# Kernel tuning notes

Measured on AMD Instinct MI355X. Metric: run time of the kernel, lower is better.

## Reference

```python
import jax, jax.numpy as jnp
import numpy as np

H = 512       # rnn_hidden_dim (enc_units == dec_units)
E = 256       # embedding_dim
V_CN = 32000  # source vocab
V_EN = 32000  # target vocab
B = 64        # batch_size
T_SRC = 64    # max_len_src
T_TRG = 64    # max_len_trg
SOS = 1


def _split3(a):
    return a[..., :H], a[..., H:2 * H], a[..., 2 * H:]


def gru_step(h, x, W, U, b):
    # Keras GRU v2 (reset_after=True), recurrent_activation=sigmoid,
    # activation='sigmoid' (non-standard; replaces tanh in candidate).
    xg = x @ W + b[0]          # [B, 3H]
    hg = h @ U + b[1]          # [B, 3H]
    xz, xr, xh = _split3(xg)
    hz, hr, hh = _split3(hg)
    z = jax.nn.sigmoid(xz + hz)
    r = jax.nn.sigmoid(xr + hr)
    hc = jax.nn.sigmoid(xh + r * hh)
    return z * h + (1.0 - z) * hc


def gru_layer(x, mask, W, U, b, reverse=False):
    # x: [B,T,D], mask: [B,T] bool. Masked steps carry state/output forward (Keras semantics).
    xt = jnp.swapaxes(x, 0, 1)
    mt = jnp.swapaxes(mask, 0, 1)
    if reverse:
        xt = xt[::-1]
        mt = mt[::-1]
    h0 = jnp.zeros((x.shape[0], H), x.dtype)

    def step(h, inp):
        xi, mi = inp
        hn = gru_step(h, xi, W, U, b)
        h = jnp.where(mi[:, None], hn, h)
        return h, h

    hT, ys = jax.lax.scan(step, h0, (xt, mt))
    if reverse:
        ys = ys[::-1]
    return jnp.swapaxes(ys, 0, 1), hT


def setup_inputs() -> dict:
    key = jax.random.key(0)
    ks = iter(jax.random.split(key, 40))

    def p(shape, s=0.05):
        return jax.random.normal(next(ks), shape, jnp.float32) * s

    inp = {
        'src': jax.random.randint(next(ks), (B, T_SRC), 0, V_CN, jnp.int32),
        'trg': jax.random.randint(next(ks), (B, T_TRG), 0, V_EN, jnp.int32),
        # encoder
        'emb_cn': p((V_CN, E)),
        'Wf': p((E, 3 * H)), 'Uf': p((H, 3 * H)), 'bf': p((2, 3 * H)),
        'Wb': p((E, 3 * H)), 'Ub': p((H, 3 * H)), 'bb': p((2, 3 * H)),
        'Wm': p((2 * H, 3 * H)), 'Um': p((H, 3 * H)), 'bm': p((2, 3 * H)),
        'Wt': p((H, 3 * H)), 'Ut': p((H, 3 * H)), 'bt': p((2, 3 * H)),
        # decoder
        'emb_en': p((V_EN, E)),
        'aW1': p((H, H)), 'ab1': p((H,)),
        'aW2': p((H, H)), 'ab2': p((H,)),
        'aV': p((H, 1)), 'abV': p((1,)),
        'Wd': p((H + E, 3 * H)), 'Ud': p((H, 3 * H)), 'bd': p((2, 3 * H)),
        'fcW': p((H, V_EN)), 'fcb': p((V_EN,)),
    }
    return inp


def reference(src, trg, emb_cn, Wf, Uf, bf, Wb, Ub, bb, Wm, Um, bm, Wt, Ut, bt,
              emb_en, aW1, ab1, aW2, ab2, aV, abV, Wd, Ud, bd, fcW, fcb):
    mask = src != 0
    x = emb_cn[src]                                    # [B,T,E]
    yf, _ = gru_layer(x, mask, Wf, Uf, bf)
    yb, _ = gru_layer(x, mask, Wb, Ub, bb, reverse=True)
    x = jnp.concatenate([yf, yb], axis=-1)             # bidirectional concat [B,T,2H]
    x, _ = gru_layer(x, mask, Wm, Um, bm)              # middle layer (enc_layer_num-2 == 1)
    enc_out, dec_hidden = gru_layer(x, mask, Wt, Ut, bt)  # [B,T,H], [B,H]

    keys = enc_out @ aW1 + ab1                         # W1(values), constant across steps [B,T,H]

    # decoder inputs: SOS then teacher-forced trg[:,1:T-1]; targets trg[:,1:]
    dec_inp = jnp.concatenate(
        [jnp.full((B, 1), SOS, jnp.int32), trg[:, 1:T_TRG - 1]], axis=1)  # [B, T-1]
    tgts = trg[:, 1:]                                                     # [B, T-1]

    def step(h, inp):
        tok, tgt = inp
        # Bahdanau attention with query = previous decoder state
        score = jnp.tanh(keys + (h @ aW2 + ab2)[:, None, :]) @ aV + abV   # [B,T,1]
        w = jax.nn.softmax(score, axis=1)
        ctx = jnp.sum(w * enc_out, axis=1)                                # [B,H]
        xin = jnp.concatenate([ctx, emb_en[tok]], axis=-1)                # [B,H+E]
        # original calls self.rnn(x) with NO initial state -> GRU starts from zeros each step
        hn = gru_step(jnp.zeros((B, H), jnp.float32), xin, Wd, Ud, bd)
        logits = hn @ fcW + fcb                                           # [B,V]
        ll = jax.nn.log_softmax(logits, axis=-1)
        ce = -jnp.take_along_axis(ll, tgt[:, None], axis=-1)[:, 0]
        l = jnp.sum(ce * (tgt != 0).astype(jnp.float32))
        return hn, l

    _, losses = jax.lax.scan(step, dec_hidden, (dec_inp.T, tgts.T))
    num = jnp.sum((trg != 0).astype(jnp.float32))
    return jnp.sum(losses) / num
```

## Files before the change

kernel.cpp:

```cpp
#include <hip/hip_runtime.h>
#include <math.h>

#define HH 512
#define EE 256
#define BB 64
#define TT 64
#define VV 32000
#define H3 1536
#define TDEC 63

typedef _Float16 v2h __attribute__((ext_vector_type(2)));
typedef _Float16 v4h __attribute__((ext_vector_type(4)));
typedef _Float16 v8h __attribute__((ext_vector_type(8)));
typedef float v4f __attribute__((ext_vector_type(4)));

__device__ __forceinline__ float sigm(float x) { return 1.f / (1.f + expf(-x)); }

__global__ void k_embed(const int* __restrict__ src, const float* __restrict__ emb,
                        float* __restrict__ x) {
    int idx = blockIdx.x * 256 + threadIdx.x;
    int row = idx >> 8;
    int e = idx & 255;
    x[idx] = emb[src[row] * EE + e];
}

__global__ void k_embtok(const int* __restrict__ trg, const float* __restrict__ emb,
                         float* __restrict__ x) {
    int idx = blockIdx.x * 256 + threadIdx.x;
    int row = idx >> 8;
    int e = idx & 255;
    int t = row >> 6, b = row & 63;
    int tok = (t == 0) ? 1 : ((t < 63) ? trg[b * TT + t] : 0);
    x[idx] = emb[tok * EE + e];
}

__global__ void k_zero1536(float* __restrict__ z) {
    int i = blockIdx.x * 256 + threadIdx.x;
    if (i < 1536) z[i] = 0.f;
}

__global__ void k_cvt_h(const float4* __restrict__ src, v2h* __restrict__ dst) {
    int i = blockIdx.x * 256 + threadIdx.x;
    float4 v = src[i];
    v2h a = {(_Float16)v.x, (_Float16)v.y};
    v2h b = {(_Float16)v.z, (_Float16)v.w};
    dst[2 * i] = a;
    dst[2 * i + 1] = b;
}

__global__ __launch_bounds__(256) void k_cvt_t(const float* __restrict__ W,
                                               _Float16* __restrict__ WT, int N) {
    __shared__ _Float16 tile[64][65];
    int n0 = blockIdx.x * 64, k0 = blockIdx.y * 64;
    int t = threadIdx.x;
#pragma unroll
    for (int i = 0; i < 16; ++i) {
        int idx = i * 256 + t;
        int r = idx >> 6, c = idx & 63;
        tile[r][c] = (_Float16)W[(size_t)(k0 + r) * N + n0 + c];
    }
    __syncthreads();
#pragma unroll
    for (int i = 0; i < 16; ++i) {
        int idx = i * 256 + t;
        int r = idx >> 6, c = idx & 63;
        WT[(size_t)(n0 + r) * 512 + k0 + c] = tile[c][r];
    }
}

__global__ __launch_bounds__(256) void k_gemm128_bias(
    const float* __restrict__ A, const float* __restrict__ W,
    const float* __restrict__ bias, float* __restrict__ C,
    int N, int K) {
    __shared__ float As[8][128];
    __shared__ float Bs[8][128];
    int row0 = blockIdx.y * 128, col0 = blockIdx.x * 128;
    int tid = threadIdx.x;
    int tx = tid & 15, ty = tid >> 4;
    int ar = tid >> 1, aq = tid & 1;
    int bkk = tid >> 5, bc4 = tid & 31;
    float acc[2][2][4][4] = {};
    for (int k0 = 0; k0 < K; k0 += 8) {
        float4 av = *(const float4*)&A[(size_t)(row0 + ar) * K + k0 + aq * 4];
        float4 bv = *(const float4*)&W[(size_t)(k0 + bkk) * N + col0 + bc4 * 4];
        As[aq * 4 + 0][ar] = av.x;
        As[aq * 4 + 1][ar] = av.y;
        As[aq * 4 + 2][ar] = av.z;
        As[aq * 4 + 3][ar] = av.w;
        *(float4*)&Bs[bkk][bc4 * 4] = bv;
        __syncthreads();
#pragma unroll
        for (int kk = 0; kk < 8; ++kk) {
            float4 a0 = *(const float4*)&As[kk][ty * 4];
            float4 a1 = *(const float4*)&As[kk][64 + ty * 4];
            float4 b0 = *(const float4*)&Bs[kk][tx * 4];
            float4 b1 = *(const float4*)&Bs[kk][64 + tx * 4];
            float a_[2][4] = {{a0.x, a0.y, a0.z, a0.w}, {a1.x, a1.y, a1.z, a1.w}};
            float b_[2][4] = {{b0.x, b0.y, b0.z, b0.w}, {b1.x, b1.y, b1.z, b1.w}};
#pragma unroll
            for (int rh = 0; rh < 2; ++rh)
#pragma unroll
                for (int i = 0; i < 4; ++i)
#pragma unroll
                    for (int ch = 0; ch < 2; ++ch)
#pragma unroll
                        for (int j = 0; j < 4; ++j)
                            acc[rh][ch][i][j] = fmaf(a_[rh][i], b_[ch][j], acc[rh][ch][i][j]);
        }
        __syncthreads();
    }
#pragma unroll
    for (int rh = 0; rh < 2; ++rh)
#pragma unroll
        for (int i = 0; i < 4; ++i) {
            int row = row0 + rh * 64 + ty * 4 + i;
#pragma unroll
            for (int ch = 0; ch < 2; ++ch) {
                int c = col0 + ch * 64 + tx * 4;
                float4 bv = *(const float4*)&bias[c];
                float4 o;
                o.x = acc[rh][ch][i][0] + bv.x;
                o.y = acc[rh][ch][i][1] + bv.y;
                o.z = acc[rh][ch][i][2] + bv.z;
                o.w = acc[rh][ch][i][3] + bv.w;
                *(float4*)&C[(size_t)row * N + c] = o;
            }
        }
}

__global__ __launch_bounds__(256) void k_gemm128_bias_h(
    const float* __restrict__ A, const float* __restrict__ W,
    const float* __restrict__ bias, _Float16* __restrict__ C,
    int N, int K) {
    __shared__ float As[8][128];
    __shared__ float Bs[8][128];
    int row0 = blockIdx.y * 128, col0 = blockIdx.x * 128;
    int tid = threadIdx.x;
    int tx = tid & 15, ty = tid >> 4;
    int ar = tid >> 1, aq = tid & 1;
    int bkk = tid >> 5, bc4 = tid & 31;
    float acc[2][2][4][4] = {};
    for (int k0 = 0; k0 < K; k0 += 8) {
        float4 av = *(const float4*)&A[(size_t)(row0 + ar) * K + k0 + aq * 4];
        float4 bv = *(const float4*)&W[(size_t)(k0 + bkk) * N + col0 + bc4 * 4];
        As[aq * 4 + 0][ar] = av.x;
        As[aq * 4 + 1][ar] = av.y;
        As[aq * 4 + 2][ar] = av.z;
        As[aq * 4 + 3][ar] = av.w;
        *(float4*)&Bs[bkk][bc4 * 4] = bv;
        __syncthreads();
#pragma unroll
        for (int kk = 0; kk < 8; ++kk) {
            float4 a0 = *(const float4*)&As[kk][ty * 4];
            float4 a1 = *(const float4*)&As[kk][64 + ty * 4];
            float4 b0 = *(const float4*)&Bs[kk][tx * 4];
            float4 b1 = *(const float4*)&Bs[kk][64 + tx * 4];
            float a_[2][4] = {{a0.x, a0.y, a0.z, a0.w}, {a1.x, a1.y, a1.z, a1.w}};
            float b_[2][4] = {{b0.x, b0.y, b0.z, b0.w}, {b1.x, b1.y, b1.z, b1.w}};
#pragma unroll
            for (int rh = 0; rh < 2; ++rh)
#pragma unroll
                for (int i = 0; i < 4; ++i)
#pragma unroll
                    for (int ch = 0; ch < 2; ++ch)
#pragma unroll
                        for (int j = 0; j < 4; ++j)
                            acc[rh][ch][i][j] = fmaf(a_[rh][i], b_[ch][j], acc[rh][ch][i][j]);
        }
        __syncthreads();
    }
#pragma unroll
    for (int rh = 0; rh < 2; ++rh)
#pragma unroll
        for (int i = 0; i < 4; ++i) {
            int row = row0 + rh * 64 + ty * 4 + i;
#pragma unroll
            for (int ch = 0; ch < 2; ++ch) {
                int c = col0 + ch * 64 + tx * 4;
                float4 bv = *(const float4*)&bias[c];
                v4h o;
                o[0] = (_Float16)(acc[rh][ch][i][0] + bv.x);
                o[1] = (_Float16)(acc[rh][ch][i][1] + bv.y);
                o[2] = (_Float16)(acc[rh][ch][i][2] + bv.z);
                o[3] = (_Float16)(acc[rh][ch][i][3] + bv.w);
                *(v4h*)&C[(size_t)row * N + c] = o;
            }
        }
}

struct GruP {
    const float* xg;
    const float* hb;
    float* y;
    const float* U;
    const float* b1;
    int t, tprev, ystride, yoff;
};

__global__ __launch_bounds__(512) void k_gru5(GruP p0, GruP p1, const int* __restrict__ src,
                                              int nblk) {
    GruP p = (blockIdx.x < nblk) ? p0 : p1;
    int blk = (blockIdx.x < nblk) ? blockIdx.x : blockIdx.x - nblk;
    int bg = blk >> 4;
    int ic = blk & 15;
    int tid = threadIdx.x;
    int c = tid & 31, kh = tid >> 5;
    int i = ic * 32 + c;
    __shared__ float hs[4][512];
    __shared__ float ps[12][512];
    for (int j = tid; j < 2048; j += 512) {
        int bl = j >> 9, k = j & 511;
        hs[bl][k] = p.hb ? p.hb[(size_t)((bg * 4 + bl) * TT + p.tprev) * p.ystride + p.yoff + k]
                         : 0.f;
    }
    __syncthreads();
    float az[4] = {}, ar[4] = {}, ah[4] = {};
    const float* Up = p.U + (size_t)(kh * 32) * H3 + i;
    int ks0 = kh * 32;
#pragma unroll 8
    for (int k = 0; k < 32; ++k) {
        const float* Ur = Up + k * H3;
        float uz = Ur[0], ur = Ur[512], uh = Ur[1024];
#pragma unroll
        for (int b = 0; b < 4; ++b) {
            float h = hs[b][ks0 + k];
            az[b] = fmaf(h, uz, az[b]);
            ar[b] = fmaf(h, ur, ar[b]);
            ah[b] = fmaf(h, uh, ah[b]);
        }
    }
#pragma unroll
    for (int b = 0; b < 4; ++b) {
        ps[b][tid] = az[b];
        ps[4 + b][tid] = ar[b];
        ps[8 + b][tid] = ah[b];
    }
    __syncthreads();
    if (tid < 128) {
        int b = tid >> 5, cc = tid & 31;
        float AZ = 0.f, AR = 0.f, AH = 0.f;
        for (int q = 0; q < 16; ++q) {
            AZ += ps[b][q * 32 + cc];
            AR += ps[4 + b][q * 32 + cc];
            AH += ps[8 + b][q * 32 + cc];
        }
        int ii = ic * 32 + cc;
        int row = (bg * 4 + b) * TT + p.t;
        const float* xr = p.xg + (size_t)row * H3;
        float z = sigm(xr[ii] + AZ + p.b1[ii]);
        float r = sigm(xr[512 + ii] + AR + p.b1[512 + ii]);
        float hc = sigm(xr[1024 + ii] + r * (AH + p.b1[1024 + ii]));
        float hp = hs[b][ii];
        float hn = (src[row] != 0) ? (z * hp + (1.f - z) * hc) : hp;
        p.y[(size_t)row * p.ystride + p.yoff + ii] = hn;
    }
}

struct EncP {
    const float* xg;
    const float* xseq;
    const float* xW;
    const float* xb0;
    float* y;
    const float* U;
    const float* b1;
    int t;
    int ystride, yoff;
};

__global__ __launch_bounds__(512) void k_enc_step(EncP pm, EncP pt, const int* __restrict__ src) {
    EncP p = (blockIdx.x < 256) ? pm : pt;
    if (p.t < 0) return;
    int blk = blockIdx.x & 255;
    int bg = blk >> 4, ic = blk & 15;
    int tid = threadIdx.x;
    int c = tid & 31, kh = tid >> 5;
    int i = ic * 32 + c;
    __shared__ float hs[4][512];
    __shared__ float xs[4][512];
    __shared__ float ps[16][512];
    bool fused = (p.xg == nullptr);
    int tprev = p.t - 1;
    for (int j = tid; j < 2048; j += 512) {
        int bl = j >> 9, k = j & 511;
        hs[bl][k] = (tprev < 0) ? 0.f
            : p.y[(size_t)((bg * 4 + bl) * TT + tprev) * p.ystride + p.yoff + k];
        if (fused)
            xs[bl][k] = p.xseq[(size_t)((bg * 4 + bl) * TT + p.t) * 512 + k];
    }
    __syncthreads();
    float az[4] = {}, ar[4] = {}, ahU[4] = {}, ahW[4] = {};
    int ks0 = kh * 32;
    {
        const float* Up = p.U + (size_t)ks0 * H3 + i;
#pragma unroll 8
        for (int k = 0; k < 32; ++k) {
            const float* Ur = Up + k * H3;
            float uz = Ur[0], ur = Ur[512], uh = Ur[1024];
#pragma unroll
            for (int b = 0; b < 4; ++b) {
                float h = hs[b][ks0 + k];
                az[b] = fmaf(h, uz, az[b]);
                ar[b] = fmaf(h, ur, ar[b]);
                ahU[b] = fmaf(h, uh, ahU[b]);
            }
        }
    }
    if (fused) {
        const float* Wp = p.xW + (size_t)ks0 * H3 + i;
#pragma unroll 8
        for (int k = 0; k < 32; ++k) {
            const float* Wr = Wp + k * H3;
            float wz = Wr[0], wr = Wr[512], wh = Wr[1024];
#pragma unroll
            for (int b = 0; b < 4; ++b) {
                float x = xs[b][ks0 + k];
                az[b] = fmaf(x, wz, az[b]);
                ar[b] = fmaf(x, wr, ar[b]);
                ahW[b] = fmaf(x, wh, ahW[b]);
            }
        }
    }
#pragma unroll
    for (int b = 0; b < 4; ++b) {
        ps[b][tid] = az[b];
        ps[4 + b][tid] = ar[b];
        ps[8 + b][tid] = ahU[b];
        ps[12 + b][tid] = ahW[b];
    }
    __syncthreads();
    if (tid < 128) {
        int b = tid >> 5, cc = tid & 31;
        float AZ = 0.f, AR = 0.f, AHU = 0.f, AHW = 0.f;
        for (int q = 0; q < 16; ++q) {
            AZ += ps[b][q * 32 + cc];
            AR += ps[4 + b][q * 32 + cc];
            AHU += ps[8 + b][q * 32 + cc];
            AHW += ps[12 + b][q * 32 + cc];
        }
        int ii = ic * 32 + cc;
        int row = (bg * 4 + b) * TT + p.t;
        float xz, xr_, xh;
        if (fused) {
            xz = p.xb0[ii];
            xr_ = p.xb0[512 + ii];
            xh = AHW + p.xb0[1024 + ii];
        } else {
            const float* xr = p.xg + (size_t)row * H3;
            xz = xr[ii];
            xr_ = xr[512 + ii];
            xh = xr[1024 + ii];
        }
        float z = sigm(xz + AZ + p.b1[ii]);
        float r = sigm(xr_ + AR + p.b1[512 + ii]);
        float hc = sigm(xh + r * (AHU + p.b1[1024 + ii]));
        float hp = hs[b][ii];
        float hn = (src[row] != 0) ? (z * hp + (1.f - z) * hc) : hp;
        p.y[(size_t)row * p.ystride + p.yoff + ii] = hn;
    }
}

__global__ __launch_bounds__(512) void k_dec_all4(
    const _Float16* __restrict__ keysh, const float* __restrict__ enc,
    const _Float16* __restrict__ aW2h,
    const float* __restrict__ ab2, const float* __restrict__ aV,
    const float* __restrict__ abV,
    const _Float16* __restrict__ ENCWh,
    const _Float16* __restrict__ EMBWh,
    const float* __restrict__ b1, _Float16* __restrict__ HMATH) {
    int b = blockIdx.x;
    int tid = threadIdx.x;
    __shared__ float hsh[HH];
    __shared__ float qs[HH];
    __shared__ float sc[TT];
    __shared__ float ps[4][HH];
    hsh[tid] = enc[((size_t)(b * TT + 63)) * HH + tid];
    __syncthreads();
    float bz = b1[tid], br_ = b1[512 + tid], bh = b1[1024 + tid];
    int ng = tid & 127, kh = tid >> 7;
    const v4h* WqA = (const v4h*)(aW2h + (size_t)(kh * 128) * HH) + ng;
    const float* hpA = hsh + kh * 128;
    for (int t = 0; t < TDEC; ++t) {
        {
            v4f acc = {0.f, 0.f, 0.f, 0.f};
#pragma unroll 16
            for (int k = 0; k < 128; ++k) {
                v4h w = WqA[(size_t)k * 128];
                float h = hpA[k];
                acc[0] = fmaf(h, (float)w[0], acc[0]);
                acc[1] = fmaf(h, (float)w[1], acc[1]);
                acc[2] = fmaf(h, (float)w[2], acc[2]);
                acc[3] = fmaf(h, (float)w[3], acc[3]);
            }
            *(v4f*)&ps[kh][ng * 4] = acc;
        }
        __syncthreads();
        qs[tid] = ps[0][tid] + ps[1][tid] + ps[2][tid] + ps[3][tid] + ab2[tid];
        __syncthreads();
        {
            int s = tid >> 3, part = tid & 7;
            const v8h* kr = (const v8h*)(keysh + (size_t)(b * TT + s) * HH + part * 64);
            const float* qp = qs + part * 64;
            const float* avp = aV + part * 64;
            float p = 0.f;
#pragma unroll
            for (int h8 = 0; h8 < 8; ++h8) {
                v8h kv = kr[h8];
#pragma unroll
                for (int u = 0; u < 8; ++u)
                    p += tanhf((float)kv[u] + qp[h8 * 8 + u]) * avp[h8 * 8 + u];
            }
            p += __shfl_down(p, 1);
            p += __shfl_down(p, 2);
            p += __shfl_down(p, 4);
            if (part == 0) sc[s] = p + abV[0];
        }
        __syncthreads();
        if (tid < 64) {
            float v = sc[tid];
            float m = v;
            for (int o = 1; o < 64; o <<= 1) m = fmaxf(m, __shfl_xor(m, o));
            float e = expf(v - m);
            float su = e;
            for (int o = 1; o < 64; o <<= 1) su += __shfl_xor(su, o);
            sc[tid] = e / su;
        }
        __syncthreads();
        {
            const _Float16* EW = ENCWh + (size_t)(b * TT) * H3;
            float p0 = 0.f, p1 = 0.f, p2 = 0.f;
#pragma unroll 8
            for (int s = 0; s < TT; ++s) {
                float w = sc[s];
                const _Float16* er = EW + (size_t)s * H3;
                p0 = fmaf(w, (float)er[tid], p0);
                p1 = fmaf(w, (float)er[512 + tid], p1);
                p2 = fmaf(w, (float)er[1024 + tid], p2);
            }
            const _Float16* mr = EMBWh + (size_t)(t * BB + b) * H3;
            float z = sigm(p0 + (float)mr[tid] + bz);
            float r = sigm(p1 + (float)mr[512 + tid] + br_);
            float hc = sigm(p2 + (float)mr[1024 + tid] + r * bh);
            float hn = (1.f - z) * hc;
            HMATH[((size_t)t * BB + b) * HH + tid] = (_Float16)hn;
            hsh[tid] = hn;
        }
        __syncthreads();
    }
}

__global__ __launch_bounds__(512) void k_gemm256_ce_m(
    const _Float16* __restrict__ Ah, const _Float16* __restrict__ WT,
    const float* __restrict__ bias, const int* __restrict__ trg,
    float* __restrict__ pmax, float* __restrict__ psum, float* __restrict__ tgtl) {
    __shared__ v2h As[256][20];
    __shared__ v2h Bs[128][20];
    __shared__ float pm[256][2];
    __shared__ float ps[256][2];
    const v2h* A2 = (const v2h*)Ah;
    const v2h* W2 = (const v2h*)WT;
    int row0 = blockIdx.y * 256, col0 = blockIdx.x * 128;
    int tid = threadIdx.x;
    int l = tid & 63, wv = tid >> 6;
    int wr = wv >> 1, wc = wv & 1;
    int lr = l & 15, kb = l >> 4;
    int sr = tid >> 1, sh = tid & 1;
    int br = (tid & 255) >> 1, bh = tid & 1;
    int arow = row0 + sr;
    if (arow > 4031) arow = 4031;
    v4f acc[4][4];
#pragma unroll
    for (int i = 0; i < 4; ++i)
#pragma unroll
        for (int j = 0; j < 4; ++j) acc[i][j] = (v4f){0.f, 0.f, 0.f, 0.f};
    for (int k0 = 0; k0 < 256; k0 += 16) {
        const v8h* agp = (const v8h*)(A2 + (size_t)arow * 256 + k0 + sh * 8);
        v8h av0 = agp[0], av1 = agp[1];
        v8h bv0, bv1;
        if (tid < 256) {
            const v8h* bgp = (const v8h*)(W2 + (size_t)(col0 + br) * 256 + k0 + bh * 8);
            bv0 = bgp[0];
            bv1 = bgp[1];
        }
        __syncthreads();
        int ca0 = (sh * 2) ^ (sr & 3), ca1 = (sh * 2 + 1) ^ (sr & 3);
        *(v8h*)&As[sr][ca0 * 4] = av0;
        *(v8h*)&As[sr][ca1 * 4] = av1;
        if (tid < 256) {
            int cb0 = (bh * 2) ^ (br & 3), cb1 = (bh * 2 + 1) ^ (br & 3);
            *(v8h*)&Bs[br][cb0 * 4] = bv0;
            *(v8h*)&Bs[br][cb1 * 4] = bv1;
        }
        __syncthreads();
        v8h af[4], bf[4];
#pragma unroll
        for (int f = 0; f < 4; ++f) {
            int ra = wr * 64 + f * 16 + lr;
            int rb = wc * 64 + f * 16 + lr;
            af[f] = *(const v8h*)&As[ra][(kb ^ (ra & 3)) * 4];
            bf[f] = *(const v8h*)&Bs[rb][(kb ^ (rb & 3)) * 4];
        }
#pragma unroll
        for (int fr = 0; fr < 4; ++fr)
#pragma unroll
            for (int fc = 0; fc < 4; ++fc)
                acc[fr][fc] = __builtin_amdgcn_mfma_f32_16x16x32_f16(
                    af[fr], bf[fc], acc[fr][fc], 0, 0, 0);
    }
    float bv[4];
#pragma unroll
    for (int fc = 0; fc < 4; ++fc) bv[fc] = bias[col0 + wc * 64 + fc * 16 + lr];
#pragma unroll
    for (int fr = 0; fr < 4; ++fr) {
#pragma unroll
        for (int ri = 0; ri < 4; ++ri) {
            int rl = wr * 64 + fr * 16 + kb * 4 + ri;
            int rg = row0 + rl;
            int tdec = rg >> 6, bq = rg & 63;
            int tgt = (rg < 4032) ? trg[bq * TT + tdec + 1] : -1;
            float vv[4];
            float lm = -1e30f;
#pragma unroll
            for (int fc = 0; fc < 4; ++fc) {
                int c = col0 + wc * 64 + fc * 16 + lr;
                float v = acc[fr][fc][ri] + bv[fc];
                vv[fc] = v;
                lm = fmaxf(lm, v);
                if (c == tgt) tgtl[rg] = v;
            }
            float lsum = 0.f;
#pragma unroll
            for (int fc = 0; fc < 4; ++fc) lsum += expf(vv[fc] - lm);
            for (int o = 1; o < 16; o <<= 1) {
                float m2 = __shfl_xor(lm, o);
                float s2 = __shfl_xor(lsum, o);
                if (m2 > lm) { lsum = lsum * expf(lm - m2) + s2; lm = m2; }
                else         { lsum += s2 * expf(m2 - lm); }
            }
            if (lr == 0) { pm[rl][wc] = lm; ps[rl][wc] = lsum; }
        }
    }
    __syncthreads();
    if (tid < 256) {
        float M = -1e30f, S = 0.f;
#pragma unroll
        for (int x = 0; x < 2; ++x) {
            float m_ = pm[tid][x], s_ = ps[tid][x];
            if (m_ > M) { S = S * expf(M - m_) + s_; M = m_; }
            else        { S += s_ * expf(m_ - M); }
        }
        int rg = row0 + tid;
        if (rg < 4032) {
            pmax[(size_t)blockIdx.x * 4032 + rg] = M;
            psum[(size_t)blockIdx.x * 4032 + rg] = S;
        }
    }
}

__global__ __launch_bounds__(256) void k_merge(
    const float* __restrict__ pmax, const float* __restrict__ psum,
    const float* __restrict__ tgtl, const int* __restrict__ trg,
    float* __restrict__ blk) {
    __shared__ float pmm[4][64];
    __shared__ float pss[4][64];
    int tid = threadIdx.x;
    int r = tid & 63, q = tid >> 6;
    int row = blockIdx.x * 64 + r;
    int c0 = q * 63, c1 = (q < 3) ? (c0 + 63) : 250;
    float M = -1e30f, S = 0.f;
    for (int c = c0; c < c1; ++c) {
        float m = pmax[(size_t)c * 4032 + row], s = psum[(size_t)c * 4032 + row];
        if (m > M) { S = S * expf(M - m) + s; M = m; }
        else       { S += s * expf(m - M); }
    }
    pmm[q][r] = M;
    pss[q][r] = S;
    __syncthreads();
    if (tid < 64) {
        float M2 = -1e30f, S2 = 0.f;
        for (int q2 = 0; q2 < 4; ++q2) {
            float m = pmm[q2][tid], s = pss[q2][tid];
            if (m > M2) { S2 = S2 * expf(M2 - m) + s; M2 = m; }
            else        { S2 += s * expf(m - M2); }
        }
        int row2 = blockIdx.x * 64 + tid;
        float lse = M2 + logf(S2);
        int tdec = row2 >> 6, b = row2 & 63;
        int tgt = trg[b * TT + tdec + 1];
        float valid = (tgt != 0) ? 1.f : 0.f;
        float ce = (lse - tgtl[row2]) * valid;
        float vs = valid;
        for (int o = 32; o > 0; o >>= 1) {
            ce += __shfl_down(ce, o);
            vs += __shfl_down(vs, o);
        }
        if (tid == 0) {
            blk[blockIdx.x * 2] = ce;
            blk[blockIdx.x * 2 + 1] = vs;
        }
    }
}

__global__ void k_final(const float* __restrict__ blk, float* __restrict__ out) {
    float s0 = 0.f, s1 = 0.f;
    for (int i = 0; i < 63; ++i) { s0 += blk[2 * i]; s1 += blk[2 * i + 1]; }
    out[0] = s0 / s1;
}

extern "C" void kernel_launch(void* const* d_in, const int* in_sizes, int n_in,
                              void* d_out, int out_size, void* d_ws, size_t ws_size,
                              hipStream_t stream) {
    const int* src = (const int*)d_in[0];
    const int* trg = (const int*)d_in[1];
    const float* emb_cn = (const float*)d_in[2];
    const float* Wf = (const float*)d_in[3];
    const float* Uf = (const float*)d_in[4];
    const float* bf = (const float*)d_in[5];
    const float* Wb = (const float*)d_in[6];
    const float* Ub = (const float*)d_in[7];
    const float* bb = (const float*)d_in[8];
    const float* Wm = (const float*)d_in[9];
    const float* Um = (const float*)d_in[10];
    const float* bm = (const float*)d_in[11];
    const float* Wt = (const float*)d_in[12];
    const float* Ut = (const float*)d_in[13];
    const float* bt = (const float*)d_in[14];
    const float* emb_en = (const float*)d_in[15];
    const float* aW1 = (const float*)d_in[16];
    const float* ab1 = (const float*)d_in[17];
    const float* aW2 = (const float*)d_in[18];
    const float* ab2 = (const float*)d_in[19];
    const float* aV = (const float*)d_in[20];
    const float* abV = (const float*)d_in[21];
    const float* Wd = (const float*)d_in[22];
    const float* bd = (const float*)d_in[24];
    const float* fcW = (const float*)d_in[25];
    const float* fcb = (const float*)d_in[26];
    float* ws = (float*)d_ws;
    float* out = (float*)d_out;

    float* X_EMB = ws;
    float* XG    = ws + 1048576;
    float* X2    = ws + 7340032;
    float* XGB   = ws + 11534336;
    float* Y3    = ws + 11534336;
    float* ENC   = ws + 13631488;
    float* TGTL  = ws + 20004864;
    float* BLK   = ws + 20008896;
    float* ZB    = ws + 20009088;
    float* XTOK  = ws;
    _Float16* ENCWH = (_Float16*)(ws + 1048576);
    _Float16* AW2H  = (_Float16*)(ws + 4194304);
    _Float16* EMBWH = (_Float16*)(ws + 7340032);
    _Float16* KEYSH = (_Float16*)(ws + 15728640);
    _Float16* HMATH = (_Float16*)ws;
    float* PMAX  = ws + 1048576;
    float* PSUM  = ws + 2056576;
    _Float16* FCWT = (_Float16*)(ws + 7340032);

    k_embed<<<4096, 256, 0, stream>>>(src, emb_cn, X_EMB);

    k_gemm128_bias<<<dim3(12, 32), 256, 0, stream>>>(X_EMB, Wf, bf, XG, 1536, 256);
    k_gemm128_bias<<<dim3(12, 32), 256, 0, stream>>>(X_EMB, Wb, bb, XGB, 1536, 256);
    for (int s = 0; s < 64; ++s) {
        GruP pf{XG, s ? X2 : nullptr, X2, Uf, bf + H3, s, s - 1, 1024, 0};
        GruP pb{XGB, s ? X2 : nullptr, X2, Ub, bb + H3, 63 - s, 64 - s, 1024, 512};
        k_gru5<<<512, 512, 0, stream>>>(pf, pb, src, 256);
    }
    k_gemm128_bias<<<dim3(12, 32), 256, 0, stream>>>(X2, Wm, bm, XG, 1536, 1024);
    for (int s = 0; s <= 64; ++s) {
        EncP pm_{XG, nullptr, nullptr, nullptr, Y3, Um, bm + H3,
                 (s <= 63) ? s : -1, 512, 0};
        EncP pt_{nullptr, Y3, Wt, bt, ENC, Ut, bt + H3,
                 s - 1, 512, 0};
        k_enc_step<<<512, 512, 0, stream>>>(pm_, pt_, src);
    }
    k_gemm128_bias_h<<<dim3(4, 32), 256, 0, stream>>>(ENC, aW1, ab1, KEYSH, 512, 512);
    k_zero1536<<<6, 256, 0, stream>>>(ZB);
    k_embtok<<<4096, 256, 0, stream>>>(trg, emb_en, XTOK);
    k_gemm128_bias_h<<<dim3(12, 32), 256, 0, stream>>>(ENC, Wd, ZB, ENCWH, 1536, 512);
    k_gemm128_bias_h<<<dim3(12, 32), 256, 0, stream>>>(XTOK, Wd + (size_t)512 * H3, bd, EMBWH,
                                                       1536, 256);
    k_cvt_h<<<256, 256, 0, stream>>>((const float4*)aW2, (v2h*)AW2H);

    k_dec_all4<<<64, 512, 0, stream>>>(KEYSH, ENC, AW2H, ab2, aV, abV,
                                       ENCWH, EMBWH, bd + H3, HMATH);

    k_cvt_t<<<dim3(500, 8), 256, 0, stream>>>(fcW, FCWT, VV);
    k_gemm256_ce_m<<<dim3(250, 16), 512, 0, stream>>>(HMATH, FCWT, fcb, trg,
                                                      PMAX, PSUM, TGTL);
    k_merge<<<63, 256, 0, stream>>>(PMAX, PSUM, TGTL, trg, BLK);
    k_final<<<1, 1, 0, stream>>>(BLK, out);
}
```

Before: 3.720 ms.

## Repack encoder-gate projections into 8-wide time chunks for vectorized decoder context

Adds a transpose kernel that reorders the per-batch encoder-gate projection (ENCWH) so that 8 consecutive source timesteps for each gate column sit together. The decoder can then load them with 16-byte v8h reads instead of 64 scalar fp16 loads per column. The query matvec is also re-split into 8 k-slices with v8h weight loads and an 8-way shared-memory reduction. This costs one extra transpose kernel, a workspace region and more shared memory, in exchange for fewer, wider loads in the sequential 63-step decoder loop.

```diff
diff --git a/kernel.cpp b/kernel.cpp
--- a/kernel.cpp
+++ b/kernel.cpp
@@ -65,6 +65,27 @@
         int idx = i * 256 + t;
         int r = idx >> 6, c = idx & 63;
         WT[(size_t)(n0 + r) * 512 + k0 + c] = tile[c][r];
+    }
+}
+
+__global__ __launch_bounds__(256) void k_trans8(const _Float16* __restrict__ S,
+                                                _Float16* __restrict__ D) {
+    __shared__ _Float16 tile[64][65];
+    int j0 = blockIdx.x * 64;
+    int b = blockIdx.y;
+    int t = threadIdx.x;
+#pragma unroll
+    for (int i = 0; i < 16; ++i) {
+        int idx = i * 256 + t;
+        int r = idx >> 6, c = idx & 63;
+        tile[r][c] = S[((size_t)(b * TT + r)) * H3 + j0 + c];
+    }
+    __syncthreads();
+#pragma unroll
+    for (int i = 0; i < 16; ++i) {
+        int idx = i * 256 + t;
+        int r = idx >> 6, c = idx & 63;
+        D[(((size_t)(b * 8 + (c >> 3)) * H3) + j0 + r) * 8 + (c & 7)] = tile[c][r];
     }
 }
 
@@ -360,12 +381,12 @@
     }
 }
 
-__global__ __launch_bounds__(512) void k_dec_all4(
+__global__ __launch_bounds__(512) void k_dec_all5(
     const _Float16* __restrict__ keysh, const float* __restrict__ enc,
     const _Float16* __restrict__ aW2h,
     const float* __restrict__ ab2, const float* __restrict__ aV,
     const float* __restrict__ abV,
-    const _Float16* __restrict__ ENCWh,
+    const _Float16* __restrict__ E8,
     const _Float16* __restrict__ EMBWh,
     const float* __restrict__ b1, _Float16* __restrict__ HMATH) {
     int b = blockIdx.x;
@@ -373,29 +394,42 @@
     __shared__ float hsh[HH];
     __shared__ float qs[HH];
     __shared__ float sc[TT];
-    __shared__ float ps[4][HH];
+    __shared__ float ps[8][HH];
     hsh[tid] = enc[((size_t)(b * TT + 63)) * HH + tid];
     __syncthreads();
     float bz = b1[tid], br_ = b1[512 + tid], bh = b1[1024 + tid];
-    int ng = tid & 127, kh = tid >> 7;
-    const v4h* WqA = (const v4h*)(aW2h + (size_t)(kh * 128) * HH) + ng;
-    const float* hpA = hsh + kh * 128;
+    int ng = tid & 63, kh = tid >> 6;
+    const _Float16* WqA = aW2h + (size_t)(kh * 64) * HH + ng * 8;
+    const float* hpA = hsh + kh * 64;
     for (int t = 0; t < TDEC; ++t) {
         {
-            v4f acc = {0.f, 0.f, 0.f, 0.f};
-#pragma unroll 16
-            for (int k = 0; k < 128; ++k) {
-                v4h w = WqA[(size_t)k * 128];
+            float a0 = 0.f, a1 = 0.f, a2 = 0.f, a3 = 0.f;
+            float a4 = 0.f, a5 = 0.f, a6 = 0.f, a7 = 0.f;
+#pragma unroll 8
+            for (int k = 0; k < 64; ++k) {
+                v8h w = *(const v8h*)(WqA + (size_t)k * HH);
                 float h = hpA[k];
-                acc[0] = fmaf(h, (float)w[0], acc[0]);
-                acc[1] = fmaf(h, (float)w[1], acc[1]);
-                acc[2] = fmaf(h, (float)w[2], acc[2]);
-                acc[3] = fmaf(h, (float)w[3], acc[3]);
-            }
-            *(v4f*)&ps[kh][ng * 4] = acc;
-        }
-        __syncthreads();
-        qs[tid] = ps[0][tid] + ps[1][tid] + ps[2][tid] + ps[3][tid] + ab2[tid];
+                a0 = fmaf(h, (float)w[0], a0);
+                a1 = fmaf(h, (float)w[1], a1);
+                a2 = fmaf(h, (float)w[2], a2);
+                a3 = fmaf(h, (float)w[3], a3);
+                a4 = fmaf(h, (float)w[4], a4);
+                a5 = fmaf(h, (float)w[5], a5);
+                a6 = fmaf(h, (float)w[6], a6);
+                a7 = fmaf(h, (float)w[7], a7);
+            }
+            v4f v0 = {a0, a1, a2, a3};
+            v4f v1 = {a4, a5, a6, a7};
+            *(v4f*)&ps[kh][ng * 8] = v0;
+            *(v4f*)&ps[kh][ng * 8 + 4] = v1;
+        }
+        __syncthreads();
+        {
+            float q = ab2[tid];
+#pragma unroll
+            for (int k8 = 0; k8 < 8; ++k8) q += ps[k8][tid];
+            qs[tid] = q;
+        }
         __syncthreads();
         {
             int s = tid >> 3, part = tid & 7;
@@ -427,20 +461,26 @@
         }
         __syncthreads();
         {
-            const _Float16* EW = ENCWh + (size_t)(b * TT) * H3;
-            float p0 = 0.f, p1 = 0.f, p2 = 0.f;
-#pragma unroll 8
-            for (int s = 0; s < TT; ++s) {
-                float w = sc[s];
-                const _Float16* er = EW + (size_t)s * H3;
-                p0 = fmaf(w, (float)er[tid], p0);
-                p1 = fmaf(w, (float)er[512 + tid], p1);
-                p2 = fmaf(w, (float)er[1024 + tid], p2);
+            float pr[3];
+#pragma unroll
+            for (int g = 0; g < 3; ++g) {
+                int j = g * 512 + tid;
+                float pg = 0.f;
+#pragma unroll
+                for (int c8 = 0; c8 < 8; ++c8) {
+                    v8h ev = *(const v8h*)(E8 + (((size_t)(b * 8 + c8) * H3) + j) * 8);
+                    const float* sp = sc + c8 * 8;
+                    pg += sp[0] * (float)ev[0] + sp[1] * (float)ev[1]
+                        + sp[2] * (float)ev[2] + sp[3] * (float)ev[3]
+                        + sp[4] * (float)ev[4] + sp[5] * (float)ev[5]
+                        + sp[6] * (float)ev[6] + sp[7] * (float)ev[7];
+                }
+                pr[g] = pg;
             }
             const _Float16* mr = EMBWh + (size_t)(t * BB + b) * H3;
-            float z = sigm(p0 + (float)mr[tid] + bz);
-            float r = sigm(p1 + (float)mr[512 + tid] + br_);
-            float hc = sigm(p2 + (float)mr[1024 + tid] + r * bh);
+            float z = sigm(pr[0] + (float)mr[tid] + bz);
+            float r = sigm(pr[1] + (float)mr[512 + tid] + br_);
+            float hc = sigm(pr[2] + (float)mr[1024 + tid] + r * bh);
             float hn = (1.f - z) * hc;
             HMATH[((size_t)t * BB + b) * HH + tid] = (_Float16)hn;
             hsh[tid] = hn;
@@ -652,6 +692,7 @@
     _Float16* ENCWH = (_Float16*)(ws + 1048576);
     _Float16* AW2H  = (_Float16*)(ws + 4194304);
     _Float16* EMBWH = (_Float16*)(ws + 7340032);
+    _Float16* E8    = (_Float16*)(ws + 10485760);
     _Float16* KEYSH = (_Float16*)(ws + 15728640);
     _Float16* HMATH = (_Float16*)ws;
     float* PMAX  = ws + 1048576;
@@ -682,9 +723,10 @@
     k_gemm128_bias_h<<<dim3(12, 32), 256, 0, stream>>>(XTOK, Wd + (size_t)512 * H3, bd, EMBWH,
                                                        1536, 256);
     k_cvt_h<<<256, 256, 0, stream>>>((const float4*)aW2, (v2h*)AW2H);
-
-    k_dec_all4<<<64, 512, 0, stream>>>(KEYSH, ENC, AW2H, ab2, aV, abV,
-                                       ENCWH, EMBWH, bd + H3, HMATH);
+    k_trans8<<<dim3(24, 64), 256, 0, stream>>>(ENCWH, E8);
+
+    k_dec_all5<<<64, 512, 0, stream>>>(KEYSH, ENC, AW2H, ab2, aV, abV,
+                                       E8, EMBWH, bd + H3, HMATH);
 
     k_cvt_t<<<dim3(500, 8), 256, 0, stream>>>(fcW, FCWT, VV);
     k_gemm256_ce_m<<<dim3(250, 16), 512, 0, stream>>>(HMATH, FCWT, fcb, trg,
```

Result: slower. 5.251 ms (+41.2%).
